# Performance work log

Hardware: AMD Instinct MI355X
Metric: run time of the kernel (lower is better)

The kernel has to match this reference:

```python
import jax, jax.numpy as jnp
import numpy as np

B, F, H, D, K = 16384, 4096, 512, 64, 512  # batch, feat, hidden, emb_dim, codebook size
M = H // D  # code positions per sample


def _leaky(h):
    return jnp.where(h > 0, h, 0.01 * h)


def setup_inputs() -> dict:
    key = jax.random.key(0)
    ks = jax.random.split(key, 16)
    lin = lambda k, i, o: jax.random.normal(k, (i, o), jnp.float32) * (1.0 / np.sqrt(i))
    return {
        "x": jax.random.uniform(ks[0], (B, F), jnp.float32),
        "We1": lin(ks[1], F, 256), "be1": jnp.zeros((256,), jnp.float32),
        "We2": lin(ks[2], 256, 128), "be2": jnp.zeros((128,), jnp.float32),
        "We3": lin(ks[3], 128, H), "be3": jnp.zeros((H,), jnp.float32),
        "Wd1": lin(ks[4], H, 128), "bd1": jnp.zeros((128,), jnp.float32),
        "Wd2": lin(ks[5], 128, 256), "bd2": jnp.zeros((256,), jnp.float32),
        "Wd3": lin(ks[6], 256, F), "bd3": jnp.zeros((F,), jnp.float32),
        "codebook": jax.random.normal(ks[7], (D, K), jnp.float32) * 0.02,  # (emb_dim, num_embeddings)
    }


def _nearest(z_e, codebook):
    # z_e: (B, D, M); codebook: (D, K). Squared-distance argmin over K.
    x2 = jnp.sum(z_e * z_e, axis=1)                       # (B, M)
    xw = jnp.einsum('bdm,dk->bmk', z_e, codebook)         # (B, M, K)
    w2 = jnp.sum(codebook * codebook, axis=0)             # (K,)
    idx = jnp.argmin(x2[..., None] - 2.0 * xw + w2, axis=-1)  # (B, M)
    quant = jnp.swapaxes(codebook.T[idx], 1, 2)           # (B, D, M)
    return quant, idx


def reference(x, We1, be1, We2, be2, We3, be3, Wd1, bd1, Wd2, bd2, Wd3, bd3, codebook):
    # encoder MLP
    h = _leaky(x @ We1 + be1)
    h = _leaky(h @ We2 + be2)
    h = _leaky(h @ We3 + be3)                             # (B, H)
    z_e = h.reshape(B, D, M)
    # emb(z_e, weight_sg=True): straight-through, weight detached
    quant_sg, idx = _nearest(z_e, jax.lax.stop_gradient(codebook))
    z_q = z_e + jax.lax.stop_gradient(quant_sg - z_e)
    # emb(z_e.detach()): grads (if any) flow to codebook via gather
    emb, _ = _nearest(jax.lax.stop_gradient(z_e), codebook)
    # decoder MLP
    g = _leaky(z_q.reshape(B, H) @ Wd1 + bd1)
    g = _leaky(g @ Wd2 + bd2)
    X_pred = jax.nn.sigmoid(g @ Wd3 + bd3)                # (B, F)
    return idx, z_e, z_q, emb, X_pred
```

## Files before the change

### kernel.cpp

```cpp
#include <hip/hip_runtime.h>
#include <cstdint>
#include <cstddef>


static constexpr int BB = 16384;
static constexpr int TM = 128, TN = 128, TK = 16;

typedef __attribute__((ext_vector_type(8))) short short8;
typedef __attribute__((ext_vector_type(8))) _Float16 half8;
typedef __attribute__((ext_vector_type(4))) float f32x4;

__device__ __forceinline__ unsigned short f2bf(float f) {
    union { float f; uint32_t u; } v; v.f = f;
    uint32_t r = (v.u + 0x7FFFu + ((v.u >> 16) & 1u)) >> 16;
    return (unsigned short)r;
}

__device__ __forceinline__ int bsw(int c) { return c + ((c >> 5) << 2); }

#define GLL16(gp, lp) \
    __builtin_amdgcn_global_load_lds( \
        (const __attribute__((address_space(1))) uint32_t*)(gp), \
        (__attribute__((address_space(3))) uint32_t*)(lp), 16, 0, 0)

__global__ __launch_bounds__(256) void gemm_fp32(
    const float* __restrict__ A, const float* __restrict__ Bm,
    const float* __restrict__ bias, float* __restrict__ C,
    float* __restrict__ part,
    int M, int N, int Kd, int kLen, int act)
{
    __shared__ float As[TK][TM + 4];
    __shared__ float Bs[TK][140];
    const int tid = threadIdx.x;
    const int bm = blockIdx.y * TM;
    const int bn = blockIdx.x * TN;
    const int kStart = blockIdx.z * kLen;
    const int tx = tid & 15;
    const int ty = tid >> 4;

    const int arow = tid >> 2;
    const int acol = (tid & 3) << 2;
    const int brow = tid >> 5;
    const int bcol = (tid & 31) << 2;

    float acc[8][8];
#pragma unroll
    for (int i = 0; i < 8; i++)
#pragma unroll
        for (int j = 0; j < 8; j++) acc[i][j] = 0.f;

    const float* Ap0 = A + (size_t)(bm + arow) * Kd + acol;
    const float* Ap1 = A + (size_t)(bm + arow + 64) * Kd + acol;
    const float* Bp0 = Bm + (size_t)brow * N + bn + bcol;
    const float* Bp1 = Bm + (size_t)(brow + 8) * N + bn + bcol;

    const int pb0 = bsw(bcol);
    const int prb0 = bsw(tx * 8);
    const int prb1 = prb0 + 4;

    for (int k0 = kStart; k0 < kStart + kLen; k0 += TK) {
        const float4 a0 = *(const float4*)(Ap0 + k0);
        const float4 a1 = *(const float4*)(Ap1 + k0);
        const float4 b0 = *(const float4*)(Bp0 + (size_t)k0 * N);
        const float4 b1 = *(const float4*)(Bp1 + (size_t)k0 * N);
        __syncthreads();
        As[acol + 0][arow] = a0.x; As[acol + 1][arow] = a0.y;
        As[acol + 2][arow] = a0.z; As[acol + 3][arow] = a0.w;
        As[acol + 0][arow + 64] = a1.x; As[acol + 1][arow + 64] = a1.y;
        As[acol + 2][arow + 64] = a1.z; As[acol + 3][arow + 64] = a1.w;
        *(float4*)&Bs[brow][pb0]     = b0;
        *(float4*)&Bs[brow + 8][pb0] = b1;
        __syncthreads();
#pragma unroll
        for (int kk = 0; kk < TK; kk++) {
            float a[8], b[8];
            *(float4*)&a[0] = *(const float4*)&As[kk][ty * 8];
            *(float4*)&a[4] = *(const float4*)&As[kk][ty * 8 + 4];
            *(float4*)&b[0] = *(const float4*)&Bs[kk][prb0];
            *(float4*)&b[4] = *(const float4*)&Bs[kk][prb1];
#pragma unroll
            for (int i = 0; i < 8; i++)
#pragma unroll
                for (int j = 0; j < 8; j++)
                    acc[i][j] = fmaf(a[i], b[j], acc[i][j]);
        }
    }

    if (part) {
        float* P = part + (size_t)blockIdx.z * M * N;
#pragma unroll
        for (int i = 0; i < 8; i++) {
            const int row = bm + ty * 8 + i;
            *(float4*)&P[(size_t)row * N + bn + tx * 8]     = *(float4*)&acc[i][0];
            *(float4*)&P[(size_t)row * N + bn + tx * 8 + 4] = *(float4*)&acc[i][4];
        }
        return;
    }

    float bv[8];
#pragma unroll
    for (int j = 0; j < 8; j++) bv[j] = bias[bn + tx * 8 + j];
#pragma unroll
    for (int i = 0; i < 8; i++) {
        const int row = bm + ty * 8 + i;
        float o[8];
#pragma unroll
        for (int j = 0; j < 8; j++) {
            float v = acc[i][j] + bv[j];
            if (act == 0) v = (v > 0.f) ? v : 0.01f * v;
            else          v = 1.0f / (1.0f + __expf(-v));
            o[j] = v;
        }
        *(float4*)&C[(size_t)row * N + bn + tx * 8]     = *(float4*)&o[0];
        *(float4*)&C[(size_t)row * N + bn + tx * 8 + 4] = *(float4*)&o[4];
    }
}

__global__ __launch_bounds__(256) void combine_act(
    const float* __restrict__ part, int S, size_t MN,
    const float* __restrict__ bias, int N,
    float* __restrict__ outF, unsigned short* __restrict__ outB)
{
    const size_t e = ((size_t)blockIdx.x * 256 + threadIdx.x) * 4;
    if (e >= MN) return;
    float4 s = *(const float4*)(part + e);
    for (int i = 1; i < S; i++) {
        const float4 p = *(const float4*)(part + (size_t)i * MN + e);
        s.x += p.x; s.y += p.y; s.z += p.z; s.w += p.w;
    }
    const int col = (int)(e & (size_t)(N - 1));
    const float4 bv = *(const float4*)(bias + col);
    float v0 = s.x + bv.x, v1 = s.y + bv.y, v2 = s.z + bv.z, v3 = s.w + bv.w;
    v0 = (v0 > 0.f) ? v0 : 0.01f * v0;
    v1 = (v1 > 0.f) ? v1 : 0.01f * v1;
    v2 = (v2 > 0.f) ? v2 : 0.01f * v2;
    v3 = (v3 > 0.f) ? v3 : 0.01f * v3;
    if (outF) {
        float4 o; o.x = v0; o.y = v1; o.z = v2; o.w = v3;
        *(float4*)(outF + e) = o;
    } else {
        ushort4 o; o.x = f2bf(v0); o.y = f2bf(v1); o.z = f2bf(v2); o.w = f2bf(v3);
        *(ushort4*)(outB + e) = o;
    }
}

__global__ __launch_bounds__(256) void transpose_cast(
    const float* __restrict__ W, unsigned short* __restrict__ WT, int R, int Cc)
{
    __shared__ float s[32][33];
    const int tx = threadIdx.x & 31, ty = threadIdx.x >> 5;
    const int c0 = blockIdx.x * 32, r0 = blockIdx.y * 32;
#pragma unroll
    for (int i = 0; i < 4; i++)
        s[ty + i * 8][tx] = W[(size_t)(r0 + ty + i * 8) * Cc + c0 + tx];
    __syncthreads();
#pragma unroll
    for (int i = 0; i < 4; i++)
        WT[(size_t)(c0 + ty + i * 8) * R + r0 + tx] = f2bf(s[tx][ty + i * 8]);
}

__global__ __launch_bounds__(256) void transpose_split_f16(
    const float* __restrict__ W, unsigned short* __restrict__ Th,
    unsigned short* __restrict__ Tl, int R, int Cc)
{
    __shared__ float s[32][33];
    const int tx = threadIdx.x & 31, ty = threadIdx.x >> 5;
    const int c0 = blockIdx.x * 32, r0 = blockIdx.y * 32;
#pragma unroll
    for (int i = 0; i < 4; i++)
        s[ty + i * 8][tx] = W[(size_t)(r0 + ty + i * 8) * Cc + c0 + tx];
    __syncthreads();
#pragma unroll
    for (int i = 0; i < 4; i++) {
        const float f = s[tx][ty + i * 8];
        const _Float16 h = (_Float16)f;
        const float fh = (float)h;
        const _Float16 lo = (_Float16)((f - fh) * 4096.0f);
        union { _Float16 hf; unsigned short u; } ch, cl;
        ch.hf = h; cl.hf = lo;
        Th[(size_t)(c0 + ty + i * 8) * R + r0 + tx] = ch.u;
        Tl[(size_t)(c0 + ty + i * 8) * R + r0 + tx] = cl.u;
    }
}

template<int BUF>
__device__ __forceinline__ void enc1_step(
    int K0,
    const float* __restrict__ gA,
    const unsigned short* __restrict__ gBh,
    const unsigned short* __restrict__ gBl,
    short (&Ah)[2][2048], short (&Al)[2][2048],
    half8 (&bhC)[4], half8 (&bhN)[4], half8 (&blS)[4],
    f32x4& p0, f32x4& p1,
    f32x4 (&acc1)[4][4], f32x4 (&acc2)[4][4],
    int aoff, int fr0)
{
    constexpr size_t rstep = (size_t)16 * 4096;
    const int kn1 = K0 + 32, kn2 = K0 + 64;
    __syncthreads();
#pragma unroll
    for (int j = 0; j < 4; j++)
        blS[j] = *(const half8*)(gBl + (size_t)j * rstep + K0);
    if (kn1 < 2048) {
#pragma unroll
        for (int j = 0; j < 4; j++)
            bhN[j] = *(const half8*)(gBh + (size_t)j * rstep + kn1);
    }
    f32x4 f0, f1;
    if (kn2 < 2048) {
        f0 = __builtin_nontemporal_load((const f32x4*)(gA + kn2));
        f1 = __builtin_nontemporal_load((const f32x4*)(gA + kn2 + 4));
    }
    half8 ah[4];
#pragma unroll
    for (int i = 0; i < 4; i++)
        ah[i] = *(const half8*)&Ah[BUF][(i << 9) + fr0];
#pragma unroll
    for (int i = 0; i < 4; i++)
#pragma unroll
        for (int j = 0; j < 4; j++)
            acc1[i][j] = __builtin_amdgcn_mfma_f32_16x16x32_f16(
                ah[i], bhC[j], acc1[i][j], 0, 0, 0);
#pragma unroll
    for (int i = 0; i < 4; i++)
#pragma unroll
        for (int j = 0; j < 4; j++)
            acc2[i][j] = __builtin_amdgcn_mfma_f32_16x16x32_f16(
                ah[i], blS[j], acc2[i][j], 0, 0, 0);
    half8 al[4];
#pragma unroll
    for (int i = 0; i < 4; i++)
        al[i] = *(const half8*)&Al[BUF][(i << 9) + fr0];
#pragma unroll
    for (int i = 0; i < 4; i++)
#pragma unroll
        for (int j = 0; j < 4; j++)
            acc2[i][j] = __builtin_amdgcn_mfma_f32_16x16x32_f16(
                al[i], bhC[j], acc2[i][j], 0, 0, 0);
    if (kn1 < 2048) {
        float fv[8];
        *(f32x4*)&fv[0] = p0;
        *(f32x4*)&fv[4] = p1;
        union { _Float16 h[8]; short8 s; } uh, ul;
#pragma unroll
        for (int e = 0; e < 8; e++) {
            const float f = fv[e];
            const _Float16 h = (_Float16)f;
            const float fh = (float)h;
            uh.h[e] = h;
            ul.h[e] = (_Float16)((f - fh) * 4096.0f);
        }
        *(short8*)&Ah[BUF ^ 1][aoff] = uh.s;
        *(short8*)&Al[BUF ^ 1][aoff] = ul.s;
    }
    if (kn2 < 2048) { p0 = f0; p1 = f1; }
}

__global__ __launch_bounds__(256, 2) void gemm_f16x2_enc1(
    const float* __restrict__ X,
    const unsigned short* __restrict__ Bh,
    const unsigned short* __restrict__ Bl,
    float* __restrict__ part)
{
    __shared__ short Ah[2][2048];
    __shared__ short Al[2][2048];
    const int tid = threadIdx.x;
    const int l = tid & 63, w = tid >> 6;
    const int lm = l & 15, lq = l >> 4;
    const int bm = blockIdx.y * 64;
    const int kStart = blockIdx.z * 2048;

    const float* gA = X + (size_t)(bm + w * 16 + lm) * 4096 + kStart + lq * 8;
    const unsigned short* gBh = Bh + (size_t)(w * 64 + lm) * 4096 + kStart + lq * 8;
    const unsigned short* gBl = Bl + (size_t)(w * 64 + lm) * 4096 + kStart + lq * 8;
    constexpr size_t rstep = (size_t)16 * 4096;

    const int aoff = (w << 9) + (l << 3);
    const int fr0 = (lq << 7) + (lm << 3);

    f32x4 acc1[4][4], acc2[4][4];
#pragma unroll
    for (int i = 0; i < 4; i++)
#pragma unroll
        for (int j = 0; j < 4; j++) {
            acc1[i][j] = (f32x4){0.f, 0.f, 0.f, 0.f};
            acc2[i][j] = (f32x4){0.f, 0.f, 0.f, 0.f};
        }

    half8 bhA[4], bhB[4], blS[4];
    f32x4 p0, p1;

    {
#pragma unroll
        for (int j = 0; j < 4; j++)
            bhA[j] = *(const half8*)(gBh + (size_t)j * rstep);
        f32x4 a0 = __builtin_nontemporal_load((const f32x4*)(gA));
        f32x4 a1 = __builtin_nontemporal_load((const f32x4*)(gA + 4));
        p0 = __builtin_nontemporal_load((const f32x4*)(gA + 32));
        p1 = __builtin_nontemporal_load((const f32x4*)(gA + 36));
        float fv[8];
        *(f32x4*)&fv[0] = a0;
        *(f32x4*)&fv[4] = a1;
        union { _Float16 h[8]; short8 s; } uh, ul;
#pragma unroll
        for (int e = 0; e < 8; e++) {
            const float f = fv[e];
            const _Float16 h = (_Float16)f;
            const float fh = (float)h;
            uh.h[e] = h;
            ul.h[e] = (_Float16)((f - fh) * 4096.0f);
        }
        *(short8*)&Ah[0][aoff] = uh.s;
        *(short8*)&Al[0][aoff] = ul.s;
    }

    for (int k2 = 0; k2 < 2048; k2 += 64) {
        enc1_step<0>(k2,      gA, gBh, gBl, Ah, Al, bhA, bhB, blS,
                     p0, p1, acc1, acc2, aoff, fr0);
        enc1_step<1>(k2 + 32, gA, gBh, gBl, Ah, Al, bhB, bhA, blS,
                     p0, p1, acc1, acc2, aoff, fr0);
    }

    float* P = part + (size_t)blockIdx.z * BB * 256;
    const float inv = 0.000244140625f;
#pragma unroll
    for (int i = 0; i < 4; i++)
#pragma unroll
        for (int j = 0; j < 4; j++) {
            const int col = w * 64 + j * 16 + lm;
#pragma unroll
            for (int r = 0; r < 4; r++) {
                const int row = bm + i * 16 + lq * 4 + r;
                P[(size_t)row * 256 + col] = acc1[i][j][r] + inv * acc2[i][j][r];
            }
        }
}

__global__ __launch_bounds__(256) void gemm_bf16_dec3(
    const unsigned short* __restrict__ Ag,
    const unsigned short* __restrict__ Bt,
    const float* __restrict__ bias, float* __restrict__ C)
{
    __shared__ short As[4096];
    __shared__ short Bs2[4096];
    const int tid = threadIdx.x;
    const int l = tid & 63, w = tid >> 6;
    const int lm = l & 15, lq = l >> 4;
    const int bm = blockIdx.y * 128, bn = blockIdx.x * 128;
    const int wm = (w >> 1) * 64, wn = (w & 1) * 64;

    const int t0 = w * 2, t1 = w * 2 + 1;
    const unsigned short* ga0 = Ag + (size_t)(bm + t0 * 16 + lm) * 256 + lq * 8;
    const unsigned short* ga1 = Ag + (size_t)(bm + t1 * 16 + lm) * 256 + lq * 8;
    const unsigned short* gb0 = Bt + (size_t)(bn + t0 * 16 + lm) * 256 + lq * 8;
    const unsigned short* gb1 = Bt + (size_t)(bn + t1 * 16 + lm) * 256 + lq * 8;

    f32x4 acc[4][4];
#pragma unroll
    for (int i = 0; i < 4; i++)
#pragma unroll
        for (int j = 0; j < 4; j++) acc[i][j] = (f32x4){0.f, 0.f, 0.f, 0.f};

    for (int k0 = 0; k0 < 256; k0 += 32) {
        __syncthreads();
        GLL16(ga0 + k0, &As[t0 * 512]);
        GLL16(ga1 + k0, &As[t1 * 512]);
        GLL16(gb0 + k0, &Bs2[t0 * 512]);
        GLL16(gb1 + k0, &Bs2[t1 * 512]);
        __syncthreads();
        short8 af[4], bf[4];
#pragma unroll
        for (int i = 0; i < 4; i++)
            af[i] = *(const short8*)&As[((w >> 1) * 4 + i) * 512 + lq * 128 + lm * 8];
#pragma unroll
        for (int j = 0; j < 4; j++)
            bf[j] = *(const short8*)&Bs2[((w & 1) * 4 + j) * 512 + lq * 128 + lm * 8];
#pragma unroll
        for (int i = 0; i < 4; i++)
#pragma unroll
            for (int j = 0; j < 4; j++)
                acc[i][j] = __builtin_amdgcn_mfma_f32_16x16x32_bf16(
                    af[i], bf[j], acc[i][j], 0, 0, 0);
    }

#pragma unroll
    for (int i = 0; i < 4; i++) {
#pragma unroll
        for (int j = 0; j < 4; j++) {
            const int col = bn + wn + j * 16 + lm;
            const float bv = bias[col];
#pragma unroll
            for (int r = 0; r < 4; r++) {
                const int row = bm + wm + i * 16 + lq * 4 + r;
                float v = acc[i][j][r] + bv;
                v = 1.0f / (1.0f + __expf(-v));
                C[(size_t)row * 4096 + col] = v;
            }
        }
    }
}

__global__ __launch_bounds__(512) void vq_argmin(
    const float* __restrict__ ze, const float* __restrict__ cb,
    float* __restrict__ idxf)
{
    __shared__ float cbs[64 * 512];
    __shared__ float As[64][68];
    __shared__ float w2s[512];
    const int tid = threadIdx.x;
    const int p0 = blockIdx.x * 64;

    const float4* cb4 = (const float4*)cb;
    float4* cbs4 = (float4*)cbs;
    for (int i = tid; i < 8192; i += 512) cbs4[i] = cb4[i];

    const float4* ze4 = (const float4*)(ze + (size_t)p0 * 64);
    for (int i = tid; i < 1024; i += 512) {
        float4 v = ze4[i];
        int e = i * 4;
        int bo = e >> 9, r = e & 511;
        int d = r >> 3, m = r & 7;
        *(float4*)&As[d][bo * 8 + m] = v;
    }
    __syncthreads();

    {
        float s = 0.f;
#pragma unroll
        for (int d = 0; d < 64; ++d) { float c = cbs[d * 512 + tid]; s = fmaf(c, c, s); }
        w2s[tid] = s;
    }
    __syncthreads();

    const int tx = tid & 63;
    const int ty = tid >> 6;

    float acc[8][8], x2a[8];
#pragma unroll
    for (int i = 0; i < 8; i++) {
        x2a[i] = 0.f;
#pragma unroll
        for (int j = 0; j < 8; j++) acc[i][j] = 0.f;
    }

#pragma unroll 8
    for (int kk = 0; kk < 64; ++kk) {
        float a[8], b[8];
        *(float4*)&a[0] = *(const float4*)&As[kk][ty * 8];
        *(float4*)&a[4] = *(const float4*)&As[kk][ty * 8 + 4];
        *(float4*)&b[0] = *(const float4*)&cbs[kk * 512 + tx * 8];
        *(float4*)&b[4] = *(const float4*)&cbs[kk * 512 + tx * 8 + 4];
#pragma unroll
        for (int i = 0; i < 8; i++) x2a[i] = fmaf(a[i], a[i], x2a[i]);
#pragma unroll
        for (int i = 0; i < 8; i++)
#pragma unroll
            for (int j = 0; j < 8; j++)
                acc[i][j] = fmaf(a[i], b[j], acc[i][j]);
    }

    float w2v[8];
#pragma unroll
    for (int j = 0; j < 8; j++) w2v[j] = w2s[tx * 8 + j];

#pragma unroll
    for (int i = 0; i < 8; i++) {
        float bd = 3.4e38f; int bk = 1 << 30;
#pragma unroll
        for (int j = 0; j < 8; j++) {
            float dsc = (x2a[i] - 2.0f * acc[i][j]) + w2v[j];
            if (dsc < bd) { bd = dsc; bk = tx * 8 + j; }
        }
        for (int off = 32; off > 0; off >>= 1) {
            float od = __shfl_xor(bd, off);
            int   ok = __shfl_xor(bk, off);
            if (od < bd || (od == bd && ok < bk)) { bd = od; bk = ok; }
        }
        if (tx == i) idxf[p0 + ty * 8 + i] = (float)bk;
    }
}

__global__ __launch_bounds__(256) void vq_gather(
    const float* __restrict__ ze, const float* __restrict__ idxf,
    const float* __restrict__ cb,
    float* __restrict__ zq, float* __restrict__ emb)
{
    const int t = blockIdx.x * 256 + threadIdx.x;
    const int e = t * 4;
    const int b = e >> 9, r = e & 511;
    const int d = r >> 3, m = r & 7;
    const float4 z = *(const float4*)(ze + e);
    float q[4];
#pragma unroll
    for (int c = 0; c < 4; c++) {
        int k = (int)idxf[b * 8 + m + c];
        q[c] = cb[d * 512 + k];
    }
    float4 zq4, em4;
    zq4.x = z.x + (q[0] - z.x); zq4.y = z.y + (q[1] - z.y);
    zq4.z = z.z + (q[2] - z.z); zq4.w = z.w + (q[3] - z.w);
    em4.x = q[0]; em4.y = q[1]; em4.z = q[2]; em4.w = q[3];
    *(float4*)(zq + e) = zq4;
    *(float4*)(emb + e) = em4;
}

extern "C" void kernel_launch(void* const* d_in, const int* in_sizes, int n_in,
                              void* d_out, int out_size, void* d_ws, size_t ws_size,
                              hipStream_t stream)
{
    const float* x   = (const float*)d_in[0];
    const float* We1 = (const float*)d_in[1];
    const float* be1 = (const float*)d_in[2];
    const float* We2 = (const float*)d_in[3];
    const float* be2 = (const float*)d_in[4];
    const float* We3 = (const float*)d_in[5];
    const float* be3 = (const float*)d_in[6];
    const float* Wd1 = (const float*)d_in[7];
    const float* bd1 = (const float*)d_in[8];
    const float* Wd2 = (const float*)d_in[9];
    const float* bd2 = (const float*)d_in[10];
    const float* Wd3 = (const float*)d_in[11];
    const float* bd3 = (const float*)d_in[12];
    const float* cb  = (const float*)d_in[13];

    float* out   = (float*)d_out;
    float* o_idx = out;
    float* o_ze  = o_idx + 131072;
    float* o_zq  = o_ze + 8388608;
    float* o_emb = o_zq + 8388608;
    float* o_X   = o_emb + 8388608;

    float* h1 = (float*)d_ws;
    float* h2 = h1 + (size_t)BB * 256;
    float* g1 = h1;
    unsigned short* g2b = (unsigned short*)(h1 + (size_t)BB * 128);
    unsigned short* WT  = (unsigned short*)h2;

    unsigned short* Bth = (unsigned short*)(o_X + 16777216);
    unsigned short* Btl = Bth + 1048576;

    transpose_split_f16<<<dim3(8, 128), 256, 0, stream>>>(We1, Bth, Btl, 4096, 256);
    gemm_f16x2_enc1<<<dim3(1, 256, 2), 256, 0, stream>>>(x, Bth, Btl, o_X);
    combine_act<<<4096, 256, 0, stream>>>(o_X, 2, (size_t)BB * 256, be1, 256, h1, nullptr);
    gemm_fp32<<<dim3(1, 128, 2), 256, 0, stream>>>(
        h1, We2, nullptr, nullptr, o_X, BB, 128, 256, 128, 0);
    combine_act<<<2048, 256, 0, stream>>>(o_X, 2, (size_t)BB * 128, be2, 128, h2, nullptr);
    gemm_fp32<<<dim3(4, 128, 1), 256, 0, stream>>>(
        h2, We3, be3, o_ze, nullptr, BB, 512, 128, 128, 0);

    vq_argmin<<<dim3(2048), dim3(512), 0, stream>>>(o_ze, cb, o_idx);
    vq_gather<<<dim3(8192), dim3(256), 0, stream>>>(o_ze, o_idx, cb, o_zq, o_emb);

    transpose_cast<<<dim3(128, 8), 256, 0, stream>>>(Wd3, WT, 256, 4096);

    gemm_fp32<<<dim3(1, 128, 4), 256, 0, stream>>>(
        o_zq, Wd1, nullptr, nullptr, o_X, BB, 128, 512, 128, 0);
    combine_act<<<2048, 256, 0, stream>>>(o_X, 4, (size_t)BB * 128, bd1, 128, g1, nullptr);
    gemm_fp32<<<dim3(2, 128, 2), 256, 0, stream>>>(
        g1, Wd2, nullptr, nullptr, o_X, BB, 256, 128, 64, 0);
    combine_act<<<4096, 256, 0, stream>>>(o_X, 2, (size_t)BB * 256, bd2, 256, nullptr, g2b);
    gemm_bf16_dec3<<<dim3(32, 128), 256, 0, stream>>>(g2b, WT, bd3, o_X);
}
```

Before: 1.056 ms.

## Replace FP32 SIMT GEMMs for middle layers with split-f16 MFMA GEMMs

Replaces the scalar FP32 FMA GEMM used for the encoder layers 2-3 and decoder layers 1-2 with a templated MFMA kernel. It splits both operands into high and low f16 parts, with the low part scaled by 4096, to keep near-FP32 accuracy. Bias and leaky-ReLU are fused into the epilogue, which removes the split-K partial buffers and the combine_act passes for those layers. Small weight transposes are added up front, and the split-f16 trick carries a risk of slight numerical drift compared with FP32.

```diff
diff --git a/kernel.cpp b/kernel.cpp
--- a/kernel.cpp
+++ b/kernel.cpp
@@ -4,7 +4,6 @@
 
 
 static constexpr int BB = 16384;
-static constexpr int TM = 128, TN = 128, TK = 16;
 
 typedef __attribute__((ext_vector_type(8))) short short8;
 typedef __attribute__((ext_vector_type(8))) _Float16 half8;
@@ -16,105 +15,10 @@
     return (unsigned short)r;
 }
 
-__device__ __forceinline__ int bsw(int c) { return c + ((c >> 5) << 2); }
-
 #define GLL16(gp, lp) \
     __builtin_amdgcn_global_load_lds( \
         (const __attribute__((address_space(1))) uint32_t*)(gp), \
         (__attribute__((address_space(3))) uint32_t*)(lp), 16, 0, 0)
-
-__global__ __launch_bounds__(256) void gemm_fp32(
-    const float* __restrict__ A, const float* __restrict__ Bm,
-    const float* __restrict__ bias, float* __restrict__ C,
-    float* __restrict__ part,
-    int M, int N, int Kd, int kLen, int act)
-{
-    __shared__ float As[TK][TM + 4];
-    __shared__ float Bs[TK][140];
-    const int tid = threadIdx.x;
-    const int bm = blockIdx.y * TM;
-    const int bn = blockIdx.x * TN;
-    const int kStart = blockIdx.z * kLen;
-    const int tx = tid & 15;
-    const int ty = tid >> 4;
-
-    const int arow = tid >> 2;
-    const int acol = (tid & 3) << 2;
-    const int brow = tid >> 5;
-    const int bcol = (tid & 31) << 2;
-
-    float acc[8][8];
-#pragma unroll
-    for (int i = 0; i < 8; i++)
-#pragma unroll
-        for (int j = 0; j < 8; j++) acc[i][j] = 0.f;
-
-    const float* Ap0 = A + (size_t)(bm + arow) * Kd + acol;
-    const float* Ap1 = A + (size_t)(bm + arow + 64) * Kd + acol;
-    const float* Bp0 = Bm + (size_t)brow * N + bn + bcol;
-    const float* Bp1 = Bm + (size_t)(brow + 8) * N + bn + bcol;
-
-    const int pb0 = bsw(bcol);
-    const int prb0 = bsw(tx * 8);
-    const int prb1 = prb0 + 4;
-
-    for (int k0 = kStart; k0 < kStart + kLen; k0 += TK) {
-        const float4 a0 = *(const float4*)(Ap0 + k0);
-        const float4 a1 = *(const float4*)(Ap1 + k0);
-        const float4 b0 = *(const float4*)(Bp0 + (size_t)k0 * N);
-        const float4 b1 = *(const float4*)(Bp1 + (size_t)k0 * N);
-        __syncthreads();
-        As[acol + 0][arow] = a0.x; As[acol + 1][arow] = a0.y;
-        As[acol + 2][arow] = a0.z; As[acol + 3][arow] = a0.w;
-        As[acol + 0][arow + 64] = a1.x; As[acol + 1][arow + 64] = a1.y;
-        As[acol + 2][arow + 64] = a1.z; As[acol + 3][arow + 64] = a1.w;
-        *(float4*)&Bs[brow][pb0]     = b0;
-        *(float4*)&Bs[brow + 8][pb0] = b1;
-        __syncthreads();
-#pragma unroll
-        for (int kk = 0; kk < TK; kk++) {
-            float a[8], b[8];
-            *(float4*)&a[0] = *(const float4*)&As[kk][ty * 8];
-            *(float4*)&a[4] = *(const float4*)&As[kk][ty * 8 + 4];
-            *(float4*)&b[0] = *(const float4*)&Bs[kk][prb0];
-            *(float4*)&b[4] = *(const float4*)&Bs[kk][prb1];
-#pragma unroll
-            for (int i = 0; i < 8; i++)
-#pragma unroll
-                for (int j = 0; j < 8; j++)
-                    acc[i][j] = fmaf(a[i], b[j], acc[i][j]);
-        }
-    }
-
-    if (part) {
-        float* P = part + (size_t)blockIdx.z * M * N;
-#pragma unroll
-        for (int i = 0; i < 8; i++) {
-            const int row = bm + ty * 8 + i;
-            *(float4*)&P[(size_t)row * N + bn + tx * 8]     = *(float4*)&acc[i][0];
-            *(float4*)&P[(size_t)row * N + bn + tx * 8 + 4] = *(float4*)&acc[i][4];
-        }
-        return;
-    }
-
-    float bv[8];
-#pragma unroll
-    for (int j = 0; j < 8; j++) bv[j] = bias[bn + tx * 8 + j];
-#pragma unroll
-    for (int i = 0; i < 8; i++) {
-        const int row = bm + ty * 8 + i;
-        float o[8];
-#pragma unroll
-        for (int j = 0; j < 8; j++) {
-            float v = acc[i][j] + bv[j];
-            if (act == 0) v = (v > 0.f) ? v : 0.01f * v;
-            else          v = 1.0f / (1.0f + __expf(-v));
-            o[j] = v;
-        }
-        *(float4*)&C[(size_t)row * N + bn + tx * 8]     = *(float4*)&o[0];
-        *(float4*)&C[(size_t)row * N + bn + tx * 8 + 4] = *(float4*)&o[4];
-    }
-}
 
 __global__ __launch_bounds__(256) void combine_act(
     const float* __restrict__ part, int S, size_t MN,
@@ -332,6 +236,165 @@
             for (int r = 0; r < 4; r++) {
                 const int row = bm + i * 16 + lq * 4 + r;
                 P[(size_t)row * 256 + col] = acc1[i][j][r] + inv * acc2[i][j][r];
+            }
+        }
+}
+
+template<int BUF, int NJ, int KLEN>
+__device__ __forceinline__ void mid_step(
+    int K0,
+    const float* __restrict__ gA,
+    const unsigned short* __restrict__ gBh,
+    const unsigned short* __restrict__ gBl,
+    short (&Ah)[2][2048], short (&Al)[2][2048],
+    half8 (&bhC)[NJ], half8 (&bhN)[NJ], half8 (&blS)[NJ],
+    f32x4& p0, f32x4& p1,
+    f32x4 (&acc1)[4][NJ], f32x4 (&acc2)[4][NJ],
+    int aoff, int fr0)
+{
+    constexpr size_t rstep = (size_t)16 * KLEN;
+    const int kn1 = K0 + 32, kn2 = K0 + 64;
+    __syncthreads();
+#pragma unroll
+    for (int j = 0; j < NJ; j++)
+        blS[j] = *(const half8*)(gBl + (size_t)j * rstep + K0);
+    if (kn1 < KLEN) {
+#pragma unroll
+        for (int j = 0; j < NJ; j++)
+            bhN[j] = *(const half8*)(gBh + (size_t)j * rstep + kn1);
+    }
+    f32x4 f0, f1;
+    if (kn2 < KLEN) {
+        f0 = *(const f32x4*)(gA + kn2);
+        f1 = *(const f32x4*)(gA + kn2 + 4);
+    }
+    half8 ah[4];
+#pragma unroll
+    for (int i = 0; i < 4; i++)
+        ah[i] = *(const half8*)&Ah[BUF][(i << 9) + fr0];
+#pragma unroll
+    for (int i = 0; i < 4; i++)
+#pragma unroll
+        for (int j = 0; j < NJ; j++)
+            acc1[i][j] = __builtin_amdgcn_mfma_f32_16x16x32_f16(
+                ah[i], bhC[j], acc1[i][j], 0, 0, 0);
+#pragma unroll
+    for (int i = 0; i < 4; i++)
+#pragma unroll
+        for (int j = 0; j < NJ; j++)
+            acc2[i][j] = __builtin_amdgcn_mfma_f32_16x16x32_f16(
+                ah[i], blS[j], acc2[i][j], 0, 0, 0);
+    half8 al[4];
+#pragma unroll
+    for (int i = 0; i < 4; i++)
+        al[i] = *(const half8*)&Al[BUF][(i << 9) + fr0];
+#pragma unroll
+    for (int i = 0; i < 4; i++)
+#pragma unroll
+        for (int j = 0; j < NJ; j++)
+            acc2[i][j] = __builtin_amdgcn_mfma_f32_16x16x32_f16(
+                al[i], bhC[j], acc2[i][j], 0, 0, 0);
+    if (kn1 < KLEN) {
+        float fv[8];
+        *(f32x4*)&fv[0] = p0;
+        *(f32x4*)&fv[4] = p1;
+        union { _Float16 h[8]; short8 s; } uh, ul;
+#pragma unroll
+        for (int e = 0; e < 8; e++) {
+            const float f = fv[e];
+            const _Float16 h = (_Float16)f;
+            const float fh = (float)h;
+            uh.h[e] = h;
+            ul.h[e] = (_Float16)((f - fh) * 4096.0f);
+        }
+        *(short8*)&Ah[BUF ^ 1][aoff] = uh.s;
+        *(short8*)&Al[BUF ^ 1][aoff] = ul.s;
+    }
+    if (kn2 < KLEN) { p0 = f0; p1 = f1; }
+}
+
+template<int NJ, int KLEN, int ACT>
+__global__ __launch_bounds__(256, 2) void gemm_f16x2_mid(
+    const float* __restrict__ A,
+    const unsigned short* __restrict__ Bh,
+    const unsigned short* __restrict__ Bl,
+    const float* __restrict__ bias,
+    float* __restrict__ Cf, unsigned short* __restrict__ Cb)
+{
+    __shared__ short Ah[2][2048];
+    __shared__ short Al[2][2048];
+    const int tid = threadIdx.x;
+    const int l = tid & 63, w = tid >> 6;
+    const int lm = l & 15, lq = l >> 4;
+    const int bm = blockIdx.y * 64;
+    const int bn = blockIdx.x * (64 * NJ);
+    const int N = gridDim.x * 64 * NJ;
+
+    const float* gA = A + (size_t)(bm + w * 16 + lm) * KLEN + lq * 8;
+    const unsigned short* gBh = Bh + (size_t)(bn + w * (16 * NJ) + lm) * KLEN + lq * 8;
+    const unsigned short* gBl = Bl + (size_t)(bn + w * (16 * NJ) + lm) * KLEN + lq * 8;
+    constexpr size_t rstep = (size_t)16 * KLEN;
+
+    const int aoff = (w << 9) + (l << 3);
+    const int fr0 = (lq << 7) + (lm << 3);
+
+    f32x4 acc1[4][NJ], acc2[4][NJ];
+#pragma unroll
+    for (int i = 0; i < 4; i++)
+#pragma unroll
+        for (int j = 0; j < NJ; j++) {
+            acc1[i][j] = (f32x4){0.f, 0.f, 0.f, 0.f};
+            acc2[i][j] = (f32x4){0.f, 0.f, 0.f, 0.f};
+        }
+
+    half8 bhA[NJ], bhB[NJ], blS[NJ];
+    f32x4 p0, p1;
+
+    {
+#pragma unroll
+        for (int j = 0; j < NJ; j++)
+            bhA[j] = *(const half8*)(gBh + (size_t)j * rstep);
+        f32x4 a0 = *(const f32x4*)(gA);
+        f32x4 a1 = *(const f32x4*)(gA + 4);
+        p0 = *(const f32x4*)(gA + 32);
+        p1 = *(const f32x4*)(gA + 36);
+        float fv[8];
+        *(f32x4*)&fv[0] = a0;
+        *(f32x4*)&fv[4] = a1;
+        union { _Float16 h[8]; short8 s; } uh, ul;
+#pragma unroll
+        for (int e = 0; e < 8; e++) {
+            const float f = fv[e];
+            const _Float16 h = (_Float16)f;
+            const float fh = (float)h;
+            uh.h[e] = h;
+            ul.h[e] = (_Float16)((f - fh) * 4096.0f);
+        }
+        *(short8*)&Ah[0][aoff] = uh.s;
+        *(short8*)&Al[0][aoff] = ul.s;
+    }
+
+    for (int k2 = 0; k2 < KLEN; k2 += 64) {
+        mid_step<0, NJ, KLEN>(k2,      gA, gBh, gBl, Ah, Al, bhA, bhB, blS,
+                              p0, p1, acc1, acc2, aoff, fr0);
+        mid_step<1, NJ, KLEN>(k2 + 32, gA, gBh, gBl, Ah, Al, bhB, bhA, blS,
+                              p0, p1, acc1, acc2, aoff, fr0);
+    }
+
+    const float inv = 0.000244140625f;
+#pragma unroll
+    for (int i = 0; i < 4; i++)
+#pragma unroll
+        for (int j = 0; j < NJ; j++) {
+            const int col = bn + w * (16 * NJ) + j * 16 + lm;
+            const float bv = bias[col];
+#pragma unroll
+            for (int r = 0; r < 4; r++) {
+                const int row = bm + i * 16 + lq * 4 + r;
+                float v = acc1[i][j][r] + inv * acc2[i][j][r] + bv;
+                v = (v > 0.f) ? v : 0.01f * v;
+                if (ACT == 0) Cf[(size_t)row * N + col] = v;
+                else          Cb[(size_t)row * N + col] = f2bf(v);
             }
         }
 }
@@ -536,28 +599,38 @@
     unsigned short* g2b = (unsigned short*)(h1 + (size_t)BB * 128);
     unsigned short* WT  = (unsigned short*)h2;
 
-    unsigned short* Bth = (unsigned short*)(o_X + 16777216);
-    unsigned short* Btl = Bth + 1048576;
+    unsigned short* Bth  = (unsigned short*)(o_X + 16777216);
+    unsigned short* Btl  = Bth + 1048576;
+    unsigned short* W2h  = Btl + 1048576;
+    unsigned short* W2l  = W2h + 32768;
+    unsigned short* W3h  = W2l + 32768;
+    unsigned short* W3l  = W3h + 65536;
+    unsigned short* Wd1h = W3l + 65536;
+    unsigned short* Wd1l = Wd1h + 65536;
+    unsigned short* Wd2h = Wd1l + 65536;
+    unsigned short* Wd2l = Wd2h + 32768;
 
     transpose_split_f16<<<dim3(8, 128), 256, 0, stream>>>(We1, Bth, Btl, 4096, 256);
+    transpose_split_f16<<<dim3(4, 8),   256, 0, stream>>>(We2, W2h, W2l, 256, 128);
+    transpose_split_f16<<<dim3(16, 4),  256, 0, stream>>>(We3, W3h, W3l, 128, 512);
+    transpose_split_f16<<<dim3(4, 16),  256, 0, stream>>>(Wd1, Wd1h, Wd1l, 512, 128);
+    transpose_split_f16<<<dim3(8, 4),   256, 0, stream>>>(Wd2, Wd2h, Wd2l, 128, 256);
+
     gemm_f16x2_enc1<<<dim3(1, 256, 2), 256, 0, stream>>>(x, Bth, Btl, o_X);
     combine_act<<<4096, 256, 0, stream>>>(o_X, 2, (size_t)BB * 256, be1, 256, h1, nullptr);
-    gemm_fp32<<<dim3(1, 128, 2), 256, 0, stream>>>(
-        h1, We2, nullptr, nullptr, o_X, BB, 128, 256, 128, 0);
-    combine_act<<<2048, 256, 0, stream>>>(o_X, 2, (size_t)BB * 128, be2, 128, h2, nullptr);
-    gemm_fp32<<<dim3(4, 128, 1), 256, 0, stream>>>(
-        h2, We3, be3, o_ze, nullptr, BB, 512, 128, 128, 0);
+    gemm_f16x2_mid<2, 256, 0><<<dim3(1, 256), 256, 0, stream>>>(
+        h1, W2h, W2l, be2, h2, nullptr);
+    gemm_f16x2_mid<4, 128, 0><<<dim3(2, 256), 256, 0, stream>>>(
+        h2, W3h, W3l, be3, o_ze, nullptr);
 
     vq_argmin<<<dim3(2048), dim3(512), 0, stream>>>(o_ze, cb, o_idx);
     vq_gather<<<dim3(8192), dim3(256), 0, stream>>>(o_ze, o_idx, cb, o_zq, o_emb);
 
     transpose_cast<<<dim3(128, 8), 256, 0, stream>>>(Wd3, WT, 256, 4096);
 
-    gemm_fp32<<<dim3(1, 128, 4), 256, 0, stream>>>(
-        o_zq, Wd1, nullptr, nullptr, o_X, BB, 128, 512, 128, 0);
-    combine_act<<<2048, 256, 0, stream>>>(o_X, 4, (size_t)BB * 128, bd1, 128, g1, nullptr);
-    gemm_fp32<<<dim3(2, 128, 2), 256, 0, stream>>>(
-        g1, Wd2, nullptr, nullptr, o_X, BB, 256, 128, 64, 0);
-    combine_act<<<4096, 256, 0, stream>>>(o_X, 2, (size_t)BB * 256, bd2, 256, nullptr, g2b);
+    gemm_f16x2_mid<2, 512, 0><<<dim3(1, 256), 256, 0, stream>>>(
+        o_zq, Wd1h, Wd1l, bd1, g1, nullptr);
+    gemm_f16x2_mid<4, 128, 1><<<dim3(1, 256), 256, 0, stream>>>(
+        g1, Wd2h, Wd2l, bd2, nullptr, g2b);
     gemm_bf16_dec3<<<dim3(32, 128), 256, 0, stream>>>(g2b, WT, bd3, o_X);
 }
```

Result: faster. 980.1 us (-7.2%).
